# Kernel optimization log

Hardware: AMD Instinct MI355X
Metric: run time of the kernel (lower is better)

Reference implementation:

```python
import jax, jax.numpy as jnp
import numpy as np
from jax import lax

EPS = 1e-5
B, T, H, L, K = 64, 1024, 12, 120, 5  # batch, seq len, hidden, lstm layers, conv kernel


def _init(key, shape, scale):
    return scale * jax.random.normal(key, shape, dtype=jnp.float32)


def setup_inputs() -> dict:
    key = jax.random.key(0)
    ks = jax.random.split(key, 16)
    return {
        "x": jax.random.normal(ks[0], (B, 6, T), dtype=jnp.float32),
        "conv_acc_w": _init(ks[1], (6, 6, K), 0.3),
        "conv_acc_b": jnp.zeros((6,), jnp.float32),
        "bn1_gamma": jnp.ones((6,), jnp.float32),
        "bn1_beta": jnp.zeros((6,), jnp.float32),
        "conv_ang_w": _init(ks[2], (6, 6, K), 0.3),
        "conv_ang_b": jnp.zeros((6,), jnp.float32),
        "bn2_gamma": jnp.ones((6,), jnp.float32),
        "bn2_beta": jnp.zeros((6,), jnp.float32),
        "attn_w": _init(ks[3], (H, 6), 0.4),
        "attn_b": jnp.zeros((H,), jnp.float32),
        "lstm_wih": _init(ks[4], (L, 4 * H, H), 0.2),
        "lstm_whh": _init(ks[5], (L, 4 * H, H), 0.2),
        "lstm_bih": _init(ks[6], (L, 4 * H), 0.1),
        "lstm_bhh": _init(ks[7], (L, 4 * H), 0.1),
        "lin1_w": _init(ks[8], (H, H), 0.3),
        "lin1_b": jnp.zeros((H,), jnp.float32),
        "lin2_w": _init(ks[9], (H, H), 0.3),
        "lin2_b": jnp.zeros((H,), jnp.float32),
        "mu_w": _init(ks[10], (H, H), 0.3),
        "mu_b": jnp.zeros((H,), jnp.float32),
        "sigma_w": _init(ks[11], (H, H), 0.3),
        "sigma_b": jnp.zeros((H,), jnp.float32),
    }


def _conv1d(x, w, b):
    # x: (B, C, T) valid conv, matches nn.Conv1d
    y = lax.conv_general_dilated(x, w, (1,), "VALID", dimension_numbers=("NCH", "OIH", "NCH"))
    return y + b[None, :, None]


def _batchnorm(x, gamma, beta):
    # training-mode BatchNorm1d: biased batch stats over (N, T)
    mean = jnp.mean(x, axis=(0, 2), keepdims=True)
    var = jnp.var(x, axis=(0, 2), keepdims=True)
    return (x - mean) * lax.rsqrt(var + EPS) * gamma[None, :, None] + beta[None, :, None]


def _lstm_stack(seq_tbh, wih, whh, bias):
    # seq_tbh: (T', B, H); stacked 120-layer LSTM, torch gate order (i, f, g, o)
    b = seq_tbh.shape[1]
    h0 = jnp.zeros((b, H), seq_tbh.dtype)

    def layer(seq, p):
        w_ih, w_hh, bb = p

        def step(carry, xt):
            h, c = carry
            g = xt @ w_ih.T + h @ w_hh.T + bb  # (B, 4H)
            i, f, gg, o = jnp.split(g, 4, axis=-1)
            c_new = jax.nn.sigmoid(f) * c + jax.nn.sigmoid(i) * jnp.tanh(gg)
            h_new = jax.nn.sigmoid(o) * jnp.tanh(c_new)
            return (h_new, c_new), h_new

        (h_T, _), out = lax.scan(step, (h0, h0), seq)
        return out, h_T

    _, h_last = lax.scan(layer, seq_tbh, (wih, whh, bias))
    return h_last  # (L, B, H): final hidden state of every layer


def _forward(x, conv_acc_w, conv_acc_b, bn1_gamma, bn1_beta, conv_ang_w, conv_ang_b,
             bn2_gamma, bn2_beta, attn_w, attn_b, lstm_wih, lstm_whh, lstm_bih, lstm_bhh,
             lin1_w, lin1_b, lin2_w, lin2_b, mu_w, mu_b, sigma_w, sigma_b):
    out_acc = jax.nn.relu(_batchnorm(_conv1d(x, conv_acc_w, conv_acc_b), bn1_gamma, bn1_beta))
    out_ang = jax.nn.relu(_batchnorm(_conv1d(out_acc, conv_ang_w, conv_ang_b), bn2_gamma, bn2_beta))
    feat = jax.nn.relu(jnp.einsum("bct,hc->bth", out_ang, attn_w) + attn_b)  # (B, T-8, H)
    seq = jnp.transpose(feat, (1, 0, 2))  # (T', B, H) time-major for scan
    h_last = _lstm_stack(seq, lstm_wih, lstm_whh, lstm_bih + lstm_bhh)
    h = jnp.transpose(h_last, (1, 0, 2))  # (B, L, H) == hidden_state.permute(1,0,2)
    h = jax.nn.relu(h @ lin1_w.T + lin1_b)
    out = jax.nn.relu(h @ lin2_w.T + lin2_b)
    mu = out @ mu_w.T + mu_b
    log_var = jax.nn.softplus(out @ sigma_w.T + sigma_b)
    return out, mu, log_var


def reference(x, conv_acc_w, conv_acc_b, bn1_gamma, bn1_beta, conv_ang_w, conv_ang_b,
              bn2_gamma, bn2_beta, attn_w, attn_b, lstm_wih, lstm_whh, lstm_bih, lstm_bhh,
              lin1_w, lin1_b, lin2_w, lin2_b, mu_w, mu_b, sigma_w, sigma_b):
    return _forward(x, conv_acc_w, conv_acc_b, bn1_gamma, bn1_beta, conv_ang_w, conv_ang_b,
                    bn2_gamma, bn2_beta, attn_w, attn_b, lstm_wih, lstm_whh, lstm_bih, lstm_bhh,
                    lin1_w, lin1_b, lin2_w, lin2_b, mu_w, mu_b, sigma_w, sigma_b)
```

## Files before the change

### kernel.cpp

```cpp
#include <hip/hip_runtime.h>
#include <math.h>

#define NLAY 120
#define TT   1016
#define NB   64
#define RB   8
#define IRS  32
#define TPB  384
#define BIGF (1 << 20)

typedef float v2f __attribute__((ext_vector_type(2)));

__device__ __forceinline__ float fast_rcp(float x) { return __builtin_amdgcn_rcpf(x); }
__device__ __forceinline__ float fast_sig(float x) { return fast_rcp(1.f + __expf(-x)); }
__device__ __forceinline__ float fast_tanh(float x) { return 1.f - 2.f * fast_rcp(1.f + __expf(2.f * x)); }

__device__ __forceinline__ int poll_ge_ag(const int* p, int tgt, int cur) {
  long g = 0;
  while (cur < tgt) {
    cur = __hip_atomic_load(p, __ATOMIC_RELAXED, __HIP_MEMORY_SCOPE_AGENT);
    if (cur >= tgt) break;
    __builtin_amdgcn_s_sleep(1);
    if (++g > 400000L) break;
  }
  return cur;
}
__device__ __forceinline__ int poll_ge_wg(const int* p, int tgt, int cur) {
  long g = 0;
  while (cur < tgt) {
    cur = __hip_atomic_load(p, __ATOMIC_RELAXED, __HIP_MEMORY_SCOPE_WORKGROUP);
    if (cur >= tgt) break;
    __builtin_amdgcn_s_sleep(1);
    if (++g > 400000L) break;
  }
  return cur;
}

__global__ void k_conv(const float* __restrict__ xin, const float* __restrict__ cw,
                       const float* __restrict__ cb, const float* __restrict__ aff,
                       float* __restrict__ yout, float* __restrict__ stat,
                       int Tin, int Tout, int use_aff)
{
  const int bx = blockIdx.x;
  const int b = bx / 6, co = bx - b * 6;
  const int tid = threadIdx.x;
  __shared__ float wsh[30];
  __shared__ float ssh[6], shsh[6];
  if (tid < 30) wsh[tid] = cw[co * 30 + tid];
  if (tid < 6) {
    ssh[tid]  = use_aff ? aff[tid] : 1.f;
    shsh[tid] = use_aff ? aff[6 + tid] : 0.f;
  }
  __syncthreads();
  const float bias = cb[co];
  float lsum = 0.f, lsq = 0.f;
  for (int t = tid; t < Tout; t += 256) {
    float acc = bias;
#pragma unroll
    for (int ci = 0; ci < 6; ++ci) {
      const float* xr = xin + ((size_t)b * 6 + ci) * Tin + t;
      const float s = ssh[ci], sh = shsh[ci];
#pragma unroll
      for (int k = 0; k < 5; ++k) {
        float v = xr[k];
        if (use_aff) v = fmaxf(fmaf(s, v, sh), 0.f);
        acc += wsh[ci * 5 + k] * v;
      }
    }
    yout[((size_t)b * 6 + co) * Tout + t] = acc;
    lsum += acc; lsq += acc * acc;
  }
  __shared__ float rs[256], rq[256];
  rs[tid] = lsum; rq[tid] = lsq;
  __syncthreads();
  for (int s = 128; s > 0; s >>= 1) {
    if (tid < s) { rs[tid] += rs[tid + s]; rq[tid] += rq[tid + s]; }
    __syncthreads();
  }
  if (tid == 0) { atomicAdd(&stat[co], rs[0]); atomicAdd(&stat[6 + co], rq[0]); }
}

__global__ void k_finalize(const float* __restrict__ stat,
                           const float* __restrict__ gamma, const float* __restrict__ beta,
                           float* __restrict__ aff, float invN)
{
  const int c = threadIdx.x;
  if (c < 6) {
    float mean = stat[c] * invN;
    float var  = stat[6 + c] * invN - mean * mean;
    float sc   = gamma[c] * rsqrtf(var + 1e-5f);
    aff[c]     = sc;
    aff[6 + c] = fmaf(-mean, sc, beta[c]);
  }
}

__global__ void k_attn(const float* __restrict__ y2, const float* __restrict__ aff2,
                       const float* __restrict__ aw, const float* __restrict__ ab,
                       float* __restrict__ seq0)
{
  const int t = blockIdx.x;
  const int tid = threadIdx.x;
  __shared__ float zb[6 * 64];
  if (tid < 384) {
    const int c = tid >> 6, bb = tid & 63;
    float v = y2[((size_t)bb * 6 + c) * TT + t];
    zb[c * 64 + bb] = fmaxf(fmaf(aff2[c], v, aff2[6 + c]), 0.f);
  }
  __syncthreads();
  const int b = tid / 12, j = tid - b * 12;
  float acc = ab[j];
#pragma unroll
  for (int c = 0; c < 6; ++c) acc += aw[j * 6 + c] * zb[c * 64 + b];
  seq0[(size_t)t * 768 + tid] = fmaxf(acc, 0.f);
}

__global__ __launch_bounds__(TPB, 2) void k_lstm(
    const float* __restrict__ wih, const float* __restrict__ whh,
    const float* __restrict__ bih, const float* __restrict__ bhh,
    const float* __restrict__ seq0, float* __restrict__ ring,
    int* __restrict__ prog, int* __restrict__ cons,
    float* __restrict__ hfin)
{
  const int bid  = blockIdx.x;
  const int c    = bid >> 2;
  const int seg  = bid & 3;
  const int tid  = threadIdx.x;
  const int w    = tid >> 6;
  const int lane = tid & 63;
  const int p    = lane / 12;
  const int j    = lane - p * 12;
  const bool act = (p < 5);
  const int pc   = act ? p : 0;
  const int l    = seg * 30 + w * 5 + pc;

  __shared__ __align__(16) float hloc[6][2][64];
  __shared__ __align__(16) float iring[5][IRS][12];
  __shared__ __align__(16) float xring[2][16][12];
  __shared__ __align__(16) float oring[16][12];
  __shared__ int pflag[6];
  __shared__ int cflag[8];
  float* xrf = &xring[0][0][0];

  if (tid < 6) pflag[tid] = 0;
  if (tid < 8) cflag[tid] = 0;
  hloc[w][0][lane] = 0.f; hloc[w][1][lane] = 0.f;
  __syncthreads();

  v2f wx_if[12], wx_go[12], wh_if[12], wh_go[12];
  v2f b_if = (v2f){0.f, 0.f}, b_go = (v2f){0.f, 0.f};
  if (act) {
    const float* wi = wih + l * 576;
    const float* wh = whh + l * 576;
#pragma unroll
    for (int k = 0; k < 12; ++k) {
      wx_if[k] = (v2f){ wi[(j     ) * 12 + k], wi[(j + 12) * 12 + k] };
      wx_go[k] = (v2f){ wi[(j + 24) * 12 + k], wi[(j + 36) * 12 + k] };
      wh_if[k] = (v2f){ wh[(j     ) * 12 + k], wh[(j + 12) * 12 + k] };
      wh_go[k] = (v2f){ wh[(j + 24) * 12 + k], wh[(j + 36) * 12 + k] };
    }
    const float* ba = bih + l * 48;
    const float* bb = bhh + l * 48;
    b_if = (v2f){ ba[j]      + bb[j],      ba[j + 12] + bb[j + 12] };
    b_go = (v2f){ ba[j + 24] + bb[j + 24], ba[j + 36] + bb[j + 36] };
  }

  const int hop_in  = c * 3 + seg - 1;
  const int hop_out = c * 3 + seg;
  const float* rin  = ring + (size_t)((seg > 0) ? hop_in : 0) * (RB * 192);
  float*       rout = ring + (size_t)((seg < 3) ? hop_out : 0) * (RB * 192);
  const bool is_feeder = (w == 0);
  const bool is_tailer = (w == 5) && (seg < 3);

  const int f0 = lane, f1 = lane + 64, f2 = lane + 128;
  const int s0o0 = (f0 / 12) * 768 + (f0 % 12);
  const int s0o1 = (f1 / 12) * 768 + (f1 % 12);
  const int s0o2 = (f2 / 12) * 768 + (f2 % 12);

  auto ld_batch = [&](int m, float* d) {
    if (seg == 0) {
      const float* b = seq0 + (size_t)m * 16 * 768 + c * 12;
      d[0] = b[s0o0]; d[1] = b[s0o1]; d[2] = b[s0o2];
    } else {
      const float* b = rin + (m & (RB - 1)) * 192;
      d[0] = __hip_atomic_load(b + f0, __ATOMIC_RELAXED, __HIP_MEMORY_SCOPE_AGENT);
      d[1] = __hip_atomic_load(b + f1, __ATOMIC_RELAXED, __HIP_MEMORY_SCOPE_AGENT);
      d[2] = __hip_atomic_load(b + f2, __ATOMIC_RELAXED, __HIP_MEMORY_SCOPE_AGENT);
    }
  };

  float pend[3] = {0.f, 0.f, 0.f};
  int kp = 0, kcons = 0;
  if (is_feeder) {
    if (seg > 0) kp = poll_ge_ag(&prog[hop_in], 2, 0);
    float cur[3];
    ld_batch(0, cur);
    ld_batch(1, pend);
    xrf[f0] = cur[0]; xrf[f1] = cur[1]; xrf[f2] = cur[2];
  }

  float cst = 0.f;
  int pcache = 0, ccache = 0;

  auto step = [&](int s, bool guard) __attribute__((always_inline)) {
    const int t  = s - pc;
    const int rb = (s & 1) ^ 1, wb = s & 1;

    const float* ax;
    if (p == 0) ax = (w == 0) ? (xrf + ((s >> 4) & 1) * 192 + (s & 15) * 12)
                              : (&iring[w - 1][s & (IRS - 1)][0]);
    else        ax = &hloc[w][rb][(pc == 0 ? 0 : pc - 1) * 12];
    const float* ah = &hloc[w][rb][pc * 12];

    float4 xA = ((const float4*)ax)[0], xB = ((const float4*)ax)[1], xC = ((const float4*)ax)[2];
    float4 hA = ((const float4*)ah)[0], hB = ((const float4*)ah)[1], hC = ((const float4*)ah)[2];
    float xv[12] = {xA.x,xA.y,xA.z,xA.w, xB.x,xB.y,xB.z,xB.w, xC.x,xC.y,xC.z,xC.w};
    float hv[12] = {hA.x,hA.y,hA.z,hA.w, hB.x,hB.y,hB.z,hB.w, hC.x,hC.y,hC.z,hC.w};

    v2f axif = (v2f){0.f,0.f}, axgo = (v2f){0.f,0.f};
    v2f ahif = b_if, ahgo = b_go;
#pragma unroll
    for (int k = 0; k < 12; ++k) {
      v2f xx = { xv[k], xv[k] };
      axif = __builtin_elementwise_fma(wx_if[k], xx, axif);
      axgo = __builtin_elementwise_fma(wx_go[k], xx, axgo);
    }
#pragma unroll
    for (int k = 0; k < 12; ++k) {
      v2f hh = { hv[k], hv[k] };
      ahif = __builtin_elementwise_fma(wh_if[k], hh, ahif);
      ahgo = __builtin_elementwise_fma(wh_go[k], hh, ahgo);
    }
    v2f aif = axif + ahif, ago = axgo + ahgo;
    float ig = fast_sig(aif.x);
    float fg = fast_sig(aif.y);
    float gg = fast_tanh(ago.x);
    float og = fast_sig(ago.y);

    if (!guard) {
      cst = fg * cst + ig * gg;
      float hn = og * fast_tanh(cst);
      hloc[w][wb][p * 12 + j] = hn;
      if (p == 4) {
        if (w < 5) iring[w][t & (IRS - 1)][j] = hn;
        else if (seg < 3) oring[t & 15][j] = hn;
      }
    } else {
      const bool run = act && (t >= 0) && (t < TT);
      if (run) {
        cst = fg * cst + ig * gg;
        float hn = og * fast_tanh(cst);
        hloc[w][wb][p * 12 + j] = hn;
        if (p == 4) {
          if (w < 5) iring[w][t & (IRS - 1)][j] = hn;
          else if (seg < 3) oring[t & 15][j] = hn;
        }
        if (t == TT - 1) hfin[l * 768 + c * 12 + j] = hn;
      }
    }

    if (is_tailer) {
      const int t4 = s - 4;
      if (t4 >= 0 && t4 < TT && (((t4 & 15) == 15) || t4 == TT - 1)) {
        const int m4 = t4 >> 4;
        if (kcons < m4 - (RB - 1) + 1)
          kcons = poll_ge_ag(&cons[hop_out], m4 - RB + 1, kcons);
        const float* orf = &oring[0][0];
        float o0 = orf[f0], o1 = orf[f1], o2 = orf[f2];
        float* d = rout + (m4 & (RB - 1)) * 192;
        __hip_atomic_store(d + f0, o0, __ATOMIC_RELAXED, __HIP_MEMORY_SCOPE_AGENT);
        __hip_atomic_store(d + f1, o1, __ATOMIC_RELAXED, __HIP_MEMORY_SCOPE_AGENT);
        __hip_atomic_store(d + f2, o2, __ATOMIC_RELAXED, __HIP_MEMORY_SCOPE_AGENT);
        if (lane == 0)
          __hip_atomic_store(&prog[hop_out], m4 + 1, __ATOMIC_RELEASE, __HIP_MEMORY_SCOPE_AGENT);
      }
    }
  };

  for (int s4 = 0; s4 < 1024; s4 += 4) {
    if (is_feeder && (s4 & 15) == 0) {
      const int m = s4 >> 4;
      if (m + 1 < NB) {
        float* xd = xrf + ((m + 1) & 1) * 192;
        xd[f0] = pend[0]; xd[f1] = pend[1]; xd[f2] = pend[2];
      }
      if (m + 2 < NB) {
        if (seg > 0 && kp < m + 3) kp = poll_ge_ag(&prog[hop_in], m + 3, kp);
        ld_batch(m + 2, pend);
      }
      if (seg > 0 && lane == 0)
        __hip_atomic_store(&cons[hop_in], m, __ATOMIC_RELAXED, __HIP_MEMORY_SCOPE_AGENT);
    }

    if (w > 0 && s4 < TT) {
      const int tgt = (s4 + 4 < TT) ? (s4 + 4) : TT;
      if (pcache < tgt) {
        pcache = poll_ge_wg(&pflag[w - 1], tgt, pcache);
        asm volatile("" ::: "memory");
      }
    }
    if (w < 5 && s4 >= 36) {
      const int tgt = s4 - 32;
      if (ccache < tgt) {
        ccache = poll_ge_wg(&cflag[w + 1], tgt, ccache);
        asm volatile("" ::: "memory");
      }
    }

    if (s4 >= 4 && s4 < 1012) {
      step(s4 + 0, false); step(s4 + 1, false); step(s4 + 2, false); step(s4 + 3, false);
    } else {
      step(s4 + 0, true);  step(s4 + 1, true);  step(s4 + 2, true);  step(s4 + 3, true);
    }

    if (lane == 0) {
      asm volatile("" ::: "memory");
      if (w < 5)
        __hip_atomic_store(&pflag[w], s4, __ATOMIC_RELAXED, __HIP_MEMORY_SCOPE_WORKGROUP);
      if (w > 0 && s4 + 3 < TT)
        __hip_atomic_store(&cflag[w], s4 + 4, __ATOMIC_RELAXED, __HIP_MEMORY_SCOPE_WORKGROUP);
    }
  }

  if (lane == 0) {
    asm volatile("" ::: "memory");
    if (w < 5) __hip_atomic_store(&pflag[w], BIGF, __ATOMIC_RELAXED, __HIP_MEMORY_SCOPE_WORKGROUP);
    if (w > 0) __hip_atomic_store(&cflag[w], BIGF, __ATOMIC_RELAXED, __HIP_MEMORY_SCOPE_WORKGROUP);
    if (is_feeder && seg > 0)
      __hip_atomic_store(&cons[hop_in], BIGF, __ATOMIC_RELAXED, __HIP_MEMORY_SCOPE_AGENT);
  }
}

__global__ void k_head(const float* __restrict__ hfin,
                       const float* __restrict__ w1, const float* __restrict__ b1,
                       const float* __restrict__ w2, const float* __restrict__ b2,
                       const float* __restrict__ wm, const float* __restrict__ bm,
                       const float* __restrict__ wsg, const float* __restrict__ bsg,
                       float* __restrict__ out)
{
  const int tid = threadIdx.x;
  __shared__ float s1[144], s2[144], sm[144], ss[144];
  __shared__ float v1[12], v2[12], vm[12], vs[12];
  if (tid < 144) { s1[tid] = w1[tid]; s2[tid] = w2[tid]; sm[tid] = wm[tid]; ss[tid] = wsg[tid]; }
  if (tid < 12)  { v1[tid] = b1[tid]; v2[tid] = b2[tid]; vm[tid] = bm[tid]; vs[tid] = bsg[tid]; }
  __syncthreads();
  const int r = blockIdx.x * 256 + tid;
  const int b = r / 120, l = r - b * 120;
  float h[12];
#pragma unroll
  for (int k = 0; k < 12; ++k) h[k] = hfin[l * 768 + b * 12 + k];
  float u1[12];
#pragma unroll
  for (int u = 0; u < 12; ++u) {
    float a = v1[u];
#pragma unroll
    for (int k = 0; k < 12; ++k) a += s1[u * 12 + k] * h[k];
    u1[u] = fmaxf(a, 0.f);
  }
  float u2[12];
#pragma unroll
  for (int u = 0; u < 12; ++u) {
    float a = v2[u];
#pragma unroll
    for (int k = 0; k < 12; ++k) a += s2[u * 12 + k] * u1[k];
    u2[u] = fmaxf(a, 0.f);
  }
  const size_t base = (size_t)r * 12;
#pragma unroll
  for (int u = 0; u < 12; ++u) out[base + u] = u2[u];
#pragma unroll
  for (int u = 0; u < 12; ++u) {
    float a = vm[u];
#pragma unroll
    for (int k = 0; k < 12; ++k) a += sm[u * 12 + k] * u2[k];
    out[92160 + base + u] = a;
  }
#pragma unroll
  for (int u = 0; u < 12; ++u) {
    float a = vs[u];
#pragma unroll
    for (int k = 0; k < 12; ++k) a += ss[u * 12 + k] * u2[k];
    out[184320 + base + u] = fmaxf(a, 0.f) + log1pf(expf(-fabsf(a)));
  }
}

extern "C" void kernel_launch(void* const* d_in, const int* in_sizes, int n_in,
                              void* d_out, int out_size, void* d_ws, size_t ws_size,
                              hipStream_t stream)
{
  const float* x   = (const float*)d_in[0];
  const float* c1w = (const float*)d_in[1];
  const float* c1b = (const float*)d_in[2];
  const float* g1  = (const float*)d_in[3];
  const float* be1 = (const float*)d_in[4];
  const float* c2w = (const float*)d_in[5];
  const float* c2b = (const float*)d_in[6];
  const float* g2  = (const float*)d_in[7];
  const float* be2 = (const float*)d_in[8];
  const float* aw  = (const float*)d_in[9];
  const float* ab  = (const float*)d_in[10];
  const float* wih = (const float*)d_in[11];
  const float* whh = (const float*)d_in[12];
  const float* bih = (const float*)d_in[13];
  const float* bhh = (const float*)d_in[14];
  const float* l1w = (const float*)d_in[15];
  const float* l1b = (const float*)d_in[16];
  const float* l2w = (const float*)d_in[17];
  const float* l2b = (const float*)d_in[18];
  const float* muw = (const float*)d_in[19];
  const float* mub = (const float*)d_in[20];
  const float* sgw = (const float*)d_in[21];
  const float* sgb = (const float*)d_in[22];

  float* ws    = (float*)d_ws;
  float* stat1 = ws;
  float* stat2 = ws + 12;
  float* aff1  = ws + 24;
  float* aff2  = ws + 36;
  int*   prog  = (int*)(ws + 64);
  int*   cons  = (int*)(ws + 304);
  float* y1    = ws + 576;
  float* y2    = y1 + 391680;
  float* seq0  = y2 + 390144;
  float* ring  = seq0 + 780288;
  float* hfin  = ring + (size_t)192 * RB * 192;

  hipMemsetAsync(d_ws, 0, 576 * sizeof(float), stream);

  k_conv<<<384, 256, 0, stream>>>(x, c1w, c1b, nullptr, y1, stat1, 1024, 1020, 0);
  k_finalize<<<1, 64, 0, stream>>>(stat1, g1, be1, aff1, 1.f / 65280.f);
  k_conv<<<384, 256, 0, stream>>>(y1, c2w, c2b, aff1, y2, stat2, 1020, 1016, 1);
  k_finalize<<<1, 64, 0, stream>>>(stat2, g2, be2, aff2, 1.f / 65024.f);
  k_attn<<<1016, 768, 0, stream>>>(y2, aff2, aw, ab, seq0);
  k_lstm<<<256, TPB, 0, stream>>>(wih, whh, bih, bhh, seq0, ring, prog, cons, hfin);
  k_head<<<30, 256, 0, stream>>>(hfin, l1w, l1b, l2w, l2b, muw, mub, sgw, sgb, (float*)d_out);
}
```

Measured before the change: 812.8 us.

## Repack LSTM wavefront pipeline into 16-lane layers with DPP recurrent broadcast

The layer-to-lane mapping in the wavefront-pipelined LSTM changes from 5 layers of 12 lanes per wave to 4 layers of 16 lanes per wave. Each block now runs 10 waves (40 layers), so each batch column uses 3 blocks instead of 4, which means fewer cross-block ring hops and 192 blocks in place of 256. The recurrent h·Whh product now gets h from DPP row rotations within each 16-lane group instead of LDS reads, with Whh pre-rotated per lane. The tailer handoff also moves out of the per-step lambda into the 4-step loop. In exchange, 4 of every 16 lanes do padded zero work, the per-block serial chain is longer, and register pressure rises under the new launch bounds of 640 threads and 3 blocks.

```diff
diff --git a/kernel.cpp b/kernel.cpp
--- a/kernel.cpp
+++ b/kernel.cpp
@@ -6,14 +6,23 @@
 #define NB   64
 #define RB   8
 #define IRS  32
-#define TPB  384
+#define WPB  10
+#define LPW  4
+#define TPB2 640
 #define BIGF (1 << 20)
 
 typedef float v2f __attribute__((ext_vector_type(2)));
+typedef float v4f __attribute__((ext_vector_type(4)));
 
 __device__ __forceinline__ float fast_rcp(float x) { return __builtin_amdgcn_rcpf(x); }
 __device__ __forceinline__ float fast_sig(float x) { return fast_rcp(1.f + __expf(-x)); }
 __device__ __forceinline__ float fast_tanh(float x) { return 1.f - 2.f * fast_rcp(1.f + __expf(2.f * x)); }
+
+template<int R>
+__device__ __forceinline__ float rotr(float x) {
+  return __int_as_float(__builtin_amdgcn_update_dpp(
+      0, __float_as_int(x), 0x120 + R, 0xf, 0xf, true));
+}
 
 __device__ __forceinline__ int poll_ge_ag(const int* p, int tgt, int cur) {
   long g = 0;
@@ -114,7 +123,7 @@
   seq0[(size_t)t * 768 + tid] = fmaxf(acc, 0.f);
 }
 
-__global__ __launch_bounds__(TPB, 2) void k_lstm(
+__global__ __launch_bounds__(TPB2, 3) void k_lstm(
     const float* __restrict__ wih, const float* __restrict__ whh,
     const float* __restrict__ bih, const float* __restrict__ bhh,
     const float* __restrict__ seq0, float* __restrict__ ring,
@@ -122,54 +131,68 @@
     float* __restrict__ hfin)
 {
   const int bid  = blockIdx.x;
-  const int c    = bid >> 2;
-  const int seg  = bid & 3;
+  const int c    = bid / 3;
+  const int seg  = bid - c * 3;
   const int tid  = threadIdx.x;
   const int w    = tid >> 6;
   const int lane = tid & 63;
-  const int p    = lane / 12;
-  const int j    = lane - p * 12;
-  const bool act = (p < 5);
-  const int pc   = act ? p : 0;
-  const int l    = seg * 30 + w * 5 + pc;
-
-  __shared__ __align__(16) float hloc[6][2][64];
-  __shared__ __align__(16) float iring[5][IRS][12];
+  const int p    = lane >> 4;
+  const int j    = lane & 15;
+  const bool actj = (j < 12);
+  const int l    = seg * 40 + w * 4 + p;
+
+  __shared__ __align__(16) float hloc[WPB][2][64];
+  __shared__ __align__(16) float iring[WPB - 1][IRS][12];
   __shared__ __align__(16) float xring[2][16][12];
   __shared__ __align__(16) float oring[16][12];
-  __shared__ int pflag[6];
-  __shared__ int cflag[8];
+  __shared__ int pflag[WPB];
+  __shared__ int cflag[WPB + 1];
   float* xrf = &xring[0][0][0];
 
-  if (tid < 6) pflag[tid] = 0;
-  if (tid < 8) cflag[tid] = 0;
+  if (tid < WPB) pflag[tid] = 0;
+  if (tid < WPB + 1) cflag[tid] = 0;
   hloc[w][0][lane] = 0.f; hloc[w][1][lane] = 0.f;
   __syncthreads();
 
-  v2f wx_if[12], wx_go[12], wh_if[12], wh_go[12];
+  v2f wx_if[12], wx_go[12];
+  v2f whr_if[16], whr_go[16];
   v2f b_if = (v2f){0.f, 0.f}, b_go = (v2f){0.f, 0.f};
-  if (act) {
+  {
     const float* wi = wih + l * 576;
     const float* wh = whh + l * 576;
 #pragma unroll
     for (int k = 0; k < 12; ++k) {
-      wx_if[k] = (v2f){ wi[(j     ) * 12 + k], wi[(j + 12) * 12 + k] };
-      wx_go[k] = (v2f){ wi[(j + 24) * 12 + k], wi[(j + 36) * 12 + k] };
-      wh_if[k] = (v2f){ wh[(j     ) * 12 + k], wh[(j + 12) * 12 + k] };
-      wh_go[k] = (v2f){ wh[(j + 24) * 12 + k], wh[(j + 36) * 12 + k] };
-    }
-    const float* ba = bih + l * 48;
-    const float* bb = bhh + l * 48;
-    b_if = (v2f){ ba[j]      + bb[j],      ba[j + 12] + bb[j + 12] };
-    b_go = (v2f){ ba[j + 24] + bb[j + 24], ba[j + 36] + bb[j + 36] };
-  }
-
-  const int hop_in  = c * 3 + seg - 1;
-  const int hop_out = c * 3 + seg;
+      if (actj) {
+        wx_if[k] = (v2f){ wi[(j     ) * 12 + k], wi[(j + 12) * 12 + k] };
+        wx_go[k] = (v2f){ wi[(j + 24) * 12 + k], wi[(j + 36) * 12 + k] };
+      } else {
+        wx_if[k] = (v2f){0.f, 0.f}; wx_go[k] = (v2f){0.f, 0.f};
+      }
+    }
+#pragma unroll
+    for (int r = 0; r < 16; ++r) {
+      const int kk = (j - r) & 15;
+      if (actj && kk < 12) {
+        whr_if[r] = (v2f){ wh[(j     ) * 12 + kk], wh[(j + 12) * 12 + kk] };
+        whr_go[r] = (v2f){ wh[(j + 24) * 12 + kk], wh[(j + 36) * 12 + kk] };
+      } else {
+        whr_if[r] = (v2f){0.f, 0.f}; whr_go[r] = (v2f){0.f, 0.f};
+      }
+    }
+    if (actj) {
+      const float* ba = bih + l * 48;
+      const float* bb = bhh + l * 48;
+      b_if = (v2f){ ba[j]      + bb[j],      ba[j + 12] + bb[j + 12] };
+      b_go = (v2f){ ba[j + 24] + bb[j + 24], ba[j + 36] + bb[j + 36] };
+    }
+  }
+
+  const int hop_in  = c * 2 + seg - 1;
+  const int hop_out = c * 2 + seg;
   const float* rin  = ring + (size_t)((seg > 0) ? hop_in : 0) * (RB * 192);
-  float*       rout = ring + (size_t)((seg < 3) ? hop_out : 0) * (RB * 192);
+  float*       rout = ring + (size_t)((seg < 2) ? hop_out : 0) * (RB * 192);
   const bool is_feeder = (w == 0);
-  const bool is_tailer = (w == 5) && (seg < 3);
+  const bool is_tailer = (w == WPB - 1) && (seg < 2);
 
   const int f0 = lane, f1 = lane + 64, f2 = lane + 128;
   const int s0o0 = (f0 / 12) * 768 + (f0 % 12);
@@ -198,70 +221,114 @@
     xrf[f0] = cur[0]; xrf[f1] = cur[1]; xrf[f2] = cur[2];
   }
 
-  float cst = 0.f;
+  float hn = 0.f, cst = 0.f;
   int pcache = 0, ccache = 0;
 
   auto step = [&](int s, bool guard) __attribute__((always_inline)) {
-    const int t  = s - pc;
+    const int t  = s - p;
     const int rb = (s & 1) ^ 1, wb = s & 1;
 
     const float* ax;
     if (p == 0) ax = (w == 0) ? (xrf + ((s >> 4) & 1) * 192 + (s & 15) * 12)
                               : (&iring[w - 1][s & (IRS - 1)][0]);
-    else        ax = &hloc[w][rb][(pc == 0 ? 0 : pc - 1) * 12];
-    const float* ah = &hloc[w][rb][pc * 12];
-
-    float4 xA = ((const float4*)ax)[0], xB = ((const float4*)ax)[1], xC = ((const float4*)ax)[2];
-    float4 hA = ((const float4*)ah)[0], hB = ((const float4*)ah)[1], hC = ((const float4*)ah)[2];
+    else        ax = &hloc[w][rb][(p - 1) * 16];
+    v4f xA = ((const v4f*)ax)[0], xB = ((const v4f*)ax)[1], xC = ((const v4f*)ax)[2];
     float xv[12] = {xA.x,xA.y,xA.z,xA.w, xB.x,xB.y,xB.z,xB.w, xC.x,xC.y,xC.z,xC.w};
-    float hv[12] = {hA.x,hA.y,hA.z,hA.w, hB.x,hB.y,hB.z,hB.w, hC.x,hC.y,hC.z,hC.w};
-
-    v2f axif = (v2f){0.f,0.f}, axgo = (v2f){0.f,0.f};
-    v2f ahif = b_if, ahgo = b_go;
+
+    float hv[16];
+    hv[0]  = hn;
+    hv[1]  = rotr<1>(hn);  hv[2]  = rotr<2>(hn);  hv[3]  = rotr<3>(hn);
+    hv[4]  = rotr<4>(hn);  hv[5]  = rotr<5>(hn);  hv[6]  = rotr<6>(hn);
+    hv[7]  = rotr<7>(hn);  hv[8]  = rotr<8>(hn);  hv[9]  = rotr<9>(hn);
+    hv[10] = rotr<10>(hn); hv[11] = rotr<11>(hn); hv[12] = rotr<12>(hn);
+    hv[13] = rotr<13>(hn); hv[14] = rotr<14>(hn); hv[15] = rotr<15>(hn);
+
+    v2f hia = b_if, hib = (v2f){0.f, 0.f};
+    v2f hga = b_go, hgb = (v2f){0.f, 0.f};
+#pragma unroll
+    for (int r = 0; r < 8; ++r) {
+      v2f ha = { hv[r], hv[r] }, hb = { hv[r + 8], hv[r + 8] };
+      hia = __builtin_elementwise_fma(whr_if[r],     ha, hia);
+      hga = __builtin_elementwise_fma(whr_go[r],     ha, hga);
+      hib = __builtin_elementwise_fma(whr_if[r + 8], hb, hib);
+      hgb = __builtin_elementwise_fma(whr_go[r + 8], hb, hgb);
+    }
+    v2f xif = (v2f){0.f, 0.f}, xgo = (v2f){0.f, 0.f};
 #pragma unroll
     for (int k = 0; k < 12; ++k) {
       v2f xx = { xv[k], xv[k] };
-      axif = __builtin_elementwise_fma(wx_if[k], xx, axif);
-      axgo = __builtin_elementwise_fma(wx_go[k], xx, axgo);
-    }
-#pragma unroll
-    for (int k = 0; k < 12; ++k) {
-      v2f hh = { hv[k], hv[k] };
-      ahif = __builtin_elementwise_fma(wh_if[k], hh, ahif);
-      ahgo = __builtin_elementwise_fma(wh_go[k], hh, ahgo);
-    }
-    v2f aif = axif + ahif, ago = axgo + ahgo;
-    float ig = fast_sig(aif.x);
-    float fg = fast_sig(aif.y);
-    float gg = fast_tanh(ago.x);
-    float og = fast_sig(ago.y);
+      xif = __builtin_elementwise_fma(wx_if[k], xx, xif);
+      xgo = __builtin_elementwise_fma(wx_go[k], xx, xgo);
+    }
+    v2f aif = (hia + hib) + xif;
+    v2f ago = (hga + hgb) + xgo;
+    float ig = fast_sig(aif.x), fg = fast_sig(aif.y);
+    float gg = fast_tanh(ago.x), og = fast_sig(ago.y);
 
     if (!guard) {
       cst = fg * cst + ig * gg;
-      float hn = og * fast_tanh(cst);
-      hloc[w][wb][p * 12 + j] = hn;
-      if (p == 4) {
-        if (w < 5) iring[w][t & (IRS - 1)][j] = hn;
-        else if (seg < 3) oring[t & 15][j] = hn;
+      float h2 = og * fast_tanh(cst);
+      hn = actj ? h2 : 0.f;
+      hloc[w][wb][p * 16 + j] = hn;
+      if (p == 3 && actj) {
+        if (w < WPB - 1) iring[w][t & (IRS - 1)][j] = hn;
+        else if (seg < 2) oring[t & 15][j] = hn;
       }
     } else {
-      const bool run = act && (t >= 0) && (t < TT);
+      const bool run = (t >= 0) && (t < TT);
       if (run) {
         cst = fg * cst + ig * gg;
-        float hn = og * fast_tanh(cst);
-        hloc[w][wb][p * 12 + j] = hn;
-        if (p == 4) {
-          if (w < 5) iring[w][t & (IRS - 1)][j] = hn;
-          else if (seg < 3) oring[t & 15][j] = hn;
+        float h2 = og * fast_tanh(cst);
+        hn = actj ? h2 : 0.f;
+        hloc[w][wb][p * 16 + j] = hn;
+        if (p == 3 && actj) {
+          if (w < WPB - 1) iring[w][t & (IRS - 1)][j] = hn;
+          else if (seg < 2) oring[t & 15][j] = hn;
         }
-        if (t == TT - 1) hfin[l * 768 + c * 12 + j] = hn;
-      }
+        if (t == TT - 1 && actj) hfin[l * 768 + c * 12 + j] = hn;
+      }
+    }
+  };
+
+  for (int s4 = 0; s4 < 1024; s4 += 4) {
+    if (is_feeder && (s4 & 15) == 0) {
+      const int m = s4 >> 4;
+      if (m + 1 < NB) {
+        float* xd = xrf + ((m + 1) & 1) * 192;
+        xd[f0] = pend[0]; xd[f1] = pend[1]; xd[f2] = pend[2];
+      }
+      if (m + 2 < NB) {
+        if (seg > 0 && kp < m + 3) kp = poll_ge_ag(&prog[hop_in], m + 3, kp);
+        ld_batch(m + 2, pend);
+      }
+      if (seg > 0 && lane == 0)
+        __hip_atomic_store(&cons[hop_in], m, __ATOMIC_RELAXED, __HIP_MEMORY_SCOPE_AGENT);
+    }
+
+    if (w > 0 && s4 < TT) {
+      const int tgt = (s4 + 4 < TT) ? (s4 + 4) : TT;
+      if (pcache < tgt) {
+        pcache = poll_ge_wg(&pflag[w - 1], tgt, pcache);
+        asm volatile("" ::: "memory");
+      }
+    }
+    if (w < WPB - 1 && s4 >= 32) {
+      const int tgt = s4 - 28;
+      if (ccache < tgt) {
+        ccache = poll_ge_wg(&cflag[w + 1], tgt, ccache);
+        asm volatile("" ::: "memory");
+      }
+    }
+
+    if (s4 >= 4 && s4 < 1012) {
+      step(s4 + 0, false); step(s4 + 1, false); step(s4 + 2, false); step(s4 + 3, false);
+    } else {
+      step(s4 + 0, true);  step(s4 + 1, true);  step(s4 + 2, true);  step(s4 + 3, true);
     }
 
     if (is_tailer) {
-      const int t4 = s - 4;
-      if (t4 >= 0 && t4 < TT && (((t4 & 15) == 15) || t4 == TT - 1)) {
-        const int m4 = t4 >> 4;
+      if ((((s4 & 15) == 0) && s4 >= 16) || s4 == 1016) {
+        const int m4 = (s4 - 1) >> 4;
         if (kcons < m4 - (RB - 1) + 1)
           kcons = poll_ge_ag(&cons[hop_out], m4 - RB + 1, kcons);
         const float* orf = &oring[0][0];
@@ -274,47 +341,10 @@
           __hip_atomic_store(&prog[hop_out], m4 + 1, __ATOMIC_RELEASE, __HIP_MEMORY_SCOPE_AGENT);
       }
     }
-  };
-
-  for (int s4 = 0; s4 < 1024; s4 += 4) {
-    if (is_feeder && (s4 & 15) == 0) {
-      const int m = s4 >> 4;
-      if (m + 1 < NB) {
-        float* xd = xrf + ((m + 1) & 1) * 192;
-        xd[f0] = pend[0]; xd[f1] = pend[1]; xd[f2] = pend[2];
-      }
-      if (m + 2 < NB) {
-        if (seg > 0 && kp < m + 3) kp = poll_ge_ag(&prog[hop_in], m + 3, kp);
-        ld_batch(m + 2, pend);
-      }
-      if (seg > 0 && lane == 0)
-        __hip_atomic_store(&cons[hop_in], m, __ATOMIC_RELAXED, __HIP_MEMORY_SCOPE_AGENT);
-    }
-
-    if (w > 0 && s4 < TT) {
-      const int tgt = (s4 + 4 < TT) ? (s4 + 4) : TT;
-      if (pcache < tgt) {
-        pcache = poll_ge_wg(&pflag[w - 1], tgt, pcache);
-        asm volatile("" ::: "memory");
-      }
-    }
-    if (w < 5 && s4 >= 36) {
-      const int tgt = s4 - 32;
-      if (ccache < tgt) {
-        ccache = poll_ge_wg(&cflag[w + 1], tgt, ccache);
-        asm volatile("" ::: "memory");
-      }
-    }
-
-    if (s4 >= 4 && s4 < 1012) {
-      step(s4 + 0, false); step(s4 + 1, false); step(s4 + 2, false); step(s4 + 3, false);
-    } else {
-      step(s4 + 0, true);  step(s4 + 1, true);  step(s4 + 2, true);  step(s4 + 3, true);
-    }
 
     if (lane == 0) {
       asm volatile("" ::: "memory");
-      if (w < 5)
+      if (w < WPB - 1)
         __hip_atomic_store(&pflag[w], s4, __ATOMIC_RELAXED, __HIP_MEMORY_SCOPE_WORKGROUP);
       if (w > 0 && s4 + 3 < TT)
         __hip_atomic_store(&cflag[w], s4 + 4, __ATOMIC_RELAXED, __HIP_MEMORY_SCOPE_WORKGROUP);
@@ -323,7 +353,7 @@
 
   if (lane == 0) {
     asm volatile("" ::: "memory");
-    if (w < 5) __hip_atomic_store(&pflag[w], BIGF, __ATOMIC_RELAXED, __HIP_MEMORY_SCOPE_WORKGROUP);
+    if (w < WPB - 1) __hip_atomic_store(&pflag[w], BIGF, __ATOMIC_RELAXED, __HIP_MEMORY_SCOPE_WORKGROUP);
     if (w > 0) __hip_atomic_store(&cflag[w], BIGF, __ATOMIC_RELAXED, __HIP_MEMORY_SCOPE_WORKGROUP);
     if (is_feeder && seg > 0)
       __hip_atomic_store(&cons[hop_in], BIGF, __ATOMIC_RELAXED, __HIP_MEMORY_SCOPE_AGENT);
@@ -422,7 +452,7 @@
   float* y2    = y1 + 391680;
   float* seq0  = y2 + 390144;
   float* ring  = seq0 + 780288;
-  float* hfin  = ring + (size_t)192 * RB * 192;
+  float* hfin  = ring + (size_t)128 * RB * 192;
 
   hipMemsetAsync(d_ws, 0, 576 * sizeof(float), stream);
 
@@ -431,6 +461,6 @@
   k_conv<<<384, 256, 0, stream>>>(y1, c2w, c2b, aff1, y2, stat2, 1020, 1016, 1);
   k_finalize<<<1, 64, 0, stream>>>(stat2, g2, be2, aff2, 1.f / 65024.f);
   k_attn<<<1016, 768, 0, stream>>>(y2, aff2, aw, ab, seq0);
-  k_lstm<<<256, TPB, 0, stream>>>(wih, whh, bih, bhh, seq0, ring, prog, cons, hfin);
+  k_lstm<<<192, TPB2, 0, stream>>>(wih, whh, bih, bhh, seq0, ring, prog, cons, hfin);
   k_head<<<30, 256, 0, stream>>>(hfin, l1w, l1b, l2w, l2b, muw, mub, sgw, sgb, (float*)d_out);
 }
```

Measured after the change: 1.700 ms. +109.2%, slower.
